# Kernel tuning notes

Hardware: AMD Instinct MI355X
Metric: run time of the kernel (lower is better)

The kernel has to match this reference:

```python
import jax, jax.numpy as jnp
import numpy as np

N_EMBD = 1024
N_HEAD = 16
HEAD_DIM = N_EMBD // N_HEAD  # 64
R = 8
D_STD = HEAD_DIM - R         # 56
BLOCK_SIZE = 2048
B, T = 2, 2048
NEG = -1e9


def setup_inputs() -> dict:
    key = jax.random.key(0)
    ks = jax.random.split(key, 8)
    x = jax.random.normal(ks[0], (B, T, N_EMBD), dtype=jnp.float32)
    Wqkv = jax.random.normal(ks[1], (3 * N_EMBD, N_EMBD), dtype=jnp.float32) * 0.02
    Wproj = jax.random.normal(ks[2], (N_EMBD, N_EMBD), dtype=jnp.float32) * 0.02
    W_recip = jax.random.normal(ks[3], (HEAD_DIM, R), dtype=jnp.float32) * 0.02
    # mixing weights must be positive (sqrt is taken); match init scale
    w_std = jnp.full((N_HEAD,), 0.5, dtype=jnp.float32)
    w_rec = jnp.full((N_HEAD,), 0.3, dtype=jnp.float32)  # > threshold -> all heads RA
    w_disc = jnp.full((N_HEAD,), 0.2, dtype=jnp.float32)
    d_bias = jax.random.normal(ks[4], (N_HEAD, BLOCK_SIZE), dtype=jnp.float32) * 0.02
    return {"x": x, "Wqkv": Wqkv, "Wproj": Wproj, "W_recip": W_recip,
            "w_std": w_std, "w_rec": w_rec, "w_disc": w_disc, "d_bias": d_bias}


def reference(x, Wqkv, Wproj, W_recip, w_std, w_rec, w_disc, d_bias):
    Bx, Tx, C = x.shape
    H, hd = N_HEAD, HEAD_DIM
    qkv = x @ Wqkv.T                                   # (B,T,3C)
    q, k, v = jnp.split(qkv, 3, axis=-1)
    def heads(t):
        return t.reshape(Bx, Tx, H, hd).transpose(0, 2, 1, 3)  # (B,H,T,hd)
    q, k, v = heads(q), heads(k), heads(v)
    q_low = jnp.einsum('bhtd,dr->bhtr', q, W_recip)    # (B,H,T,R)
    k_low = jnp.einsum('bhtd,dr->bhtr', k, W_recip)
    sw_std = jnp.sqrt(w_std)[None, :, None, None]
    sw_rec = jnp.sqrt(w_rec)[None, :, None, None]
    # cross augmentation: q side carries k_low, k side carries q_low
    q_aug = jnp.concatenate([sw_std * q[..., :D_STD], sw_rec * k_low], axis=-1)
    k_aug = jnp.concatenate([sw_std * k[..., :D_STD], sw_rec * q_low], axis=-1)
    scale = 1.0 / jnp.sqrt(jnp.asarray(hd, dtype=x.dtype))
    scores = jnp.einsum('bhqd,bhkd->bhqk', q_aug, k_aug) * scale
    # per-head learned bias over key positions, broadcast over queries
    bias = w_disc[None, :, None, None] * d_bias[:, :Tx][None, :, None, :]
    scores = scores + bias
    causal = jnp.tril(jnp.ones((Tx, Tx), dtype=bool))
    scores = jnp.where(causal[None, None], scores, NEG)
    attn = jax.nn.softmax(scores, axis=-1)
    out = jnp.einsum('bhqk,bhkd->bhqd', attn, v)       # (B,H,T,hd)
    out = out.transpose(0, 2, 1, 3).reshape(Bx, Tx, C)
    return out @ Wproj.T
```

## Files before the change

kernel.cpp:

```cpp
#include <hip/hip_runtime.h>
#include <math.h>

#define T_SEQ 2048
#define NH 16
#define HD 64
#define CEMB 1024
#define NEGINF -3.0e38f
#define LOG2E 1.4426950408889634f

typedef unsigned short ushort;
typedef unsigned int uint;
typedef __attribute__((ext_vector_type(8))) short short8;
typedef __attribute__((ext_vector_type(4))) float f32x4;

#if __has_builtin(__builtin_amdgcn_exp2f)
#define EXP2(x) __builtin_amdgcn_exp2f(x)
#else
#define EXP2(x) exp2f(x)
#endif

__device__ __forceinline__ float b2f(ushort h) {
    union { uint u; float f; } cv; cv.u = ((uint)h) << 16; return cv.f;
}
__device__ __forceinline__ ushort f2b(float f) {
    union { float f; uint u; } cv; cv.f = f;
    return (ushort)((cv.u + 0x7FFF + ((cv.u >> 16) & 1)) >> 16);
}
__device__ __forceinline__ ushort f2b_fast(float f) {
    union { float f; uint u; } cv; cv.f = f;
    return (ushort)((cv.u + 0x8000) >> 16);
}
__device__ __forceinline__ uint pack_bf16(float a, float b) {
    union { float f; uint u; } ua, ub; ua.f = a; ub.f = b;
    return __builtin_amdgcn_perm(ub.u + 0x8000u, ua.u + 0x8000u, 0x07060302u);
}
__device__ __forceinline__ void gl2lds16(const ushort* g, ushort* l) {
    __builtin_amdgcn_global_load_lds(
        (const __attribute__((address_space(1))) void*)g,
        (__attribute__((address_space(3))) void*)l, 16, 0, 0);
}

__global__ __launch_bounds__(256) void prep_kernel(
    const float* __restrict__ x, const float* __restrict__ Wqkv,
    const float* __restrict__ Wproj, const float* __restrict__ W_recip,
    const float* __restrict__ w_disc, const float* __restrict__ d_bias,
    ushort* __restrict__ xb, ushort* __restrict__ wqkvb,
    ushort* __restrict__ wprojb, float* __restrict__ bias_pre)
{
    const int bid = blockIdx.x;
    if (bid < 8192) {
        const float* src; ushort* dst; int off;
        if (bid < 4096)      { src = x;     dst = xb;     off = bid; }
        else if (bid < 7168) { src = Wqkv;  dst = wqkvb;  off = bid - 4096; }
        else                 { src = Wproj; dst = wprojb; off = bid - 7168; }
        const int i = (off * 256 + threadIdx.x) * 4;
        const float4 v = *(const float4*)&src[i];
        ushort4 o;
        o.x = f2b(v.x); o.y = f2b(v.y); o.z = f2b(v.z); o.w = f2b(v.w);
        *(ushort4*)&dst[i] = o;
        return;
    }
    if (bid >= 8224) {
        const int h = bid - 8224;
        const float wd = w_disc[h] * LOG2E;
        const int j = h * T_SEQ + threadIdx.x * 8;
        const float4 a = *(const float4*)&d_bias[j];
        const float4 c = *(const float4*)&d_bias[j + 4];
        float4 oa, oc;
        oa.x = a.x * wd; oa.y = a.y * wd; oa.z = a.z * wd; oa.w = a.w * wd;
        oc.x = c.x * wd; oc.y = c.y * wd; oc.z = c.z * wd; oc.w = c.w * wd;
        *(float4*)&bias_pre[j] = oa;
        *(float4*)&bias_pre[j + 4] = oc;
        return;
    }
    const int wb = bid - 8192;
    const int qk = wb >> 4, h = wb & 15;
    const int e0 = threadIdx.x * 4;
    f32x4 acc[8];
    #pragma unroll
    for (int r = 0; r < 8; ++r) acc[r] = (f32x4){0.f, 0.f, 0.f, 0.f};
    #pragma unroll 4
    for (int d = 0; d < 64; ++d) {
        const float4 xv = *(const float4*)&Wqkv[(size_t)(qk * 1024 + h * 64 + d) * 1024 + e0];
        #pragma unroll
        for (int r = 0; r < 8; ++r) {
            const float w = W_recip[d * 8 + r];
            acc[r][0] = fmaf(w, xv.x, acc[r][0]);
            acc[r][1] = fmaf(w, xv.y, acc[r][1]);
            acc[r][2] = fmaf(w, xv.z, acc[r][2]);
            acc[r][3] = fmaf(w, xv.w, acc[r][3]);
        }
    }
    #pragma unroll
    for (int r = 0; r < 8; ++r) {
        ushort4 o;
        o.x = f2b(acc[r][0]); o.y = f2b(acc[r][1]);
        o.z = f2b(acc[r][2]); o.w = f2b(acc[r][3]);
        *(ushort4*)&wqkvb[(size_t)(3072 + qk * 128 + h * 8 + r) * 1024 + e0] = o;
    }
}

#define GEMM_CORE(Aptr, Bptr, KDIM, SMEMN)                                     \
    __shared__ __align__(16) ushort SMEM[SMEMN];                               \
    ushort* const Asl = SMEM;                                                  \
    ushort* const Bsl = SMEM + 8192;                                           \
    const int row0 = blockIdx.x * 128;                                         \
    const int col0 = blockIdx.y * 128;                                         \
    const int tid = threadIdx.x;                                               \
    const int wave = tid >> 6, lane = tid & 63;                                \
    const int wm = wave >> 1, wn = wave & 1;                                   \
    const int quad = lane >> 4, lq = lane & 15;                                \
    const int l7 = lq & 7;                                                     \
    f32x4 acc[4][4];                                                           \
    _Pragma("unroll") for (int i = 0; i < 4; ++i)                              \
        _Pragma("unroll") for (int j = 0; j < 4; ++j)                          \
            acc[i][j] = (f32x4){0.f, 0.f, 0.f, 0.f};                           \
    for (int k0 = 0; k0 < (KDIM); k0 += 64) {                                  \
        _Pragma("unroll") for (int p = 0; p < 4; ++p) {                        \
            const int idx = p * 256 + tid;                                     \
            const int row = idx >> 3, slot = idx & 7;                          \
            const int kc = (slot ^ (row & 7)) << 3;                            \
            gl2lds16(&(Aptr)[(size_t)(row0 + row) * (KDIM) + k0 + kc], &Asl[idx * 8]); \
            gl2lds16(&(Bptr)[(size_t)(col0 + row) * (KDIM) + k0 + kc], &Bsl[idx * 8]); \
        }                                                                      \
        __syncthreads();                                                       \
        _Pragma("unroll") for (int ks = 0; ks < 2; ++ks) {                     \
            short8 af[4], bf[4];                                               \
            _Pragma("unroll") for (int i = 0; i < 4; ++i)                      \
                af[i] = *(const short8*)&Asl[(wm * 64 + i * 16 + lq) * 64 +    \
                                             (((ks * 4 + quad) ^ l7) << 3)];   \
            _Pragma("unroll") for (int j = 0; j < 4; ++j)                      \
                bf[j] = *(const short8*)&Bsl[(wn * 64 + j * 16 + lq) * 64 +    \
                                             (((ks * 4 + quad) ^ l7) << 3)];   \
            _Pragma("unroll") for (int i = 0; i < 4; ++i)                      \
                _Pragma("unroll") for (int j = 0; j < 4; ++j)                  \
                    acc[i][j] = __builtin_amdgcn_mfma_f32_16x16x32_bf16(       \
                        af[i], bf[j], acc[i][j], 0, 0, 0);                     \
        }                                                                      \
        __syncthreads();                                                       \
    }

#define CSTR 144
__global__ __launch_bounds__(256, 4) void gemm_qkv_kernel(
    const ushort* __restrict__ A, const ushort* __restrict__ Bt,
    const float* __restrict__ w_std, const float* __restrict__ w_rec,
    ushort* __restrict__ qh, ushort* __restrict__ kh, ushort* __restrict__ vt)
{
    GEMM_CORE(A, Bt, 1024, 128 * CSTR)
    ushort* const Cs = SMEM;

    if (col0 >= 2048 && col0 < 3072) {
        #pragma unroll
        for (int j = 0; j < 4; ++j) {
            const int cc = col0 + wn * 64 + j * 16 + lq;
            const int h = (cc >> 6) & 15;
            const int d = cc & 63;
            #pragma unroll
            for (int i = 0; i < 4; ++i) {
                const int rr0 = row0 + wm * 64 + i * 16 + quad * 4;
                const int b = rr0 >> 11, t0 = rr0 & 2047;
                ushort4 pv;
                pv.x = f2b(acc[i][j][0]); pv.y = f2b(acc[i][j][1]);
                pv.z = f2b(acc[i][j][2]); pv.w = f2b(acc[i][j][3]);
                *(ushort4*)&vt[((((size_t)b * NH + h) * HD + d) * T_SEQ + t0)] = pv;
            }
        }
    } else if (col0 < 2048) {
        const bool isq = (col0 < 1024);
        #pragma unroll
        for (int j = 0; j < 4; ++j) {
            const int colc = wn * 64 + j * 16 + lq;
            const int h = ((col0 + colc) >> 6) & 15;
            const float sc = isq ? w_std[h] * (0.125f * LOG2E) : 1.0f;
            #pragma unroll
            for (int i = 0; i < 4; ++i)
                #pragma unroll
                for (int r = 0; r < 4; ++r)
                    Cs[(wm * 64 + i * 16 + quad * 4 + r) * CSTR + colc] =
                        f2b(acc[i][j][r] * sc);
        }
        __syncthreads();
        ushort* dst = isq ? qh : kh;
        const int hbase = (col0 >> 6) & 15;
        #pragma unroll
        for (int rep = 0; rep < 8; ++rep) {
            const int id = rep * 256 + tid;
            const int row = id >> 4, chunk = id & 15;
            if ((chunk & 7) == 7) continue;
            const int h = hbase + (chunk >> 3);
            const int d = (chunk & 7) * 8;
            const int rr = row0 + row;
            const int b = rr >> 11, t = rr & 2047;
            const uint4 val = *(const uint4*)&Cs[row * CSTR + chunk * 8];
            *(uint4*)&dst[((((size_t)b * NH + h) * T_SEQ + t) * HD + d)] = val;
        }
    } else {
        const bool isqlow = (col0 < 3200);
        #pragma unroll
        for (int j = 0; j < 4; ++j) {
            const int colc = wn * 64 + j * 16 + lq;
            const int h = colc >> 3;
            const float sc = isqlow ? 1.0f : w_rec[h] * (0.125f * LOG2E);
            #pragma unroll
            for (int i = 0; i < 4; ++i)
                #pragma unroll
                for (int r = 0; r < 4; ++r)
                    Cs[(wm * 64 + i * 16 + quad * 4 + r) * CSTR + colc] =
                        f2b(acc[i][j][r] * sc);
        }
        __syncthreads();
        ushort* dst = isqlow ? kh : qh;
        #pragma unroll
        for (int rep = 0; rep < 8; ++rep) {
            const int id = rep * 256 + tid;
            const int row = id >> 4, h = id & 15;
            const int rr = row0 + row;
            const int b = rr >> 11, t = rr & 2047;
            const uint4 val = *(const uint4*)&Cs[row * CSTR + h * 8];
            *(uint4*)&dst[((((size_t)b * NH + h) * T_SEQ + t) * HD + 56)] = val;
        }
    }
}

__global__ __launch_bounds__(256, 4) void gemm_proj_kernel(
    const ushort* __restrict__ A, const ushort* __restrict__ Bt,
    float* __restrict__ C)
{
    GEMM_CORE(A, Bt, 1024, 16384)
    #pragma unroll
    for (int i = 0; i < 4; ++i) {
        #pragma unroll
        for (int r = 0; r < 4; ++r) {
            const int rr = row0 + wm * 64 + i * 16 + quad * 4 + r;
            #pragma unroll
            for (int j = 0; j < 4; ++j) {
                const int cc = col0 + wn * 64 + j * 16 + lq;
                C[(size_t)rr * 1024 + cc] = acc[i][j][r];
            }
        }
    }
}

#define TILE_COMPUTE(bq, o4, lsum, qrow, NTL) do {                            \
    f32x4 s4[8];                                                              \
    _Pragma("unroll") for (int nt = 0; nt < (NTL); ++nt)                      \
        s4[nt] = *(const f32x4*)&bias_h[k0 + nt * 16 + quad * 4];             \
    __builtin_amdgcn_s_setprio(1);                                            \
    _Pragma("unroll") for (int ks = 0; ks < 2; ++ks)                          \
        _Pragma("unroll") for (int nt = 0; nt < (NTL); ++nt) {                \
            const short8 ak = *(const short8*)                                \
                &Ks[(nt * 16 + lq) * 64 + (((ks * 4 + quad) ^ l7) << 3)];     \
            s4[nt] = __builtin_amdgcn_mfma_f32_16x16x32_bf16(                 \
                ak, (bq)[ks], s4[nt], 0, 0, 0);                               \
        }                                                                     \
    __builtin_amdgcn_s_setprio(0);                                            \
    _Pragma("unroll") for (int nt = 0; nt < (NTL); ++nt) {                    \
        f32x4 sv = s4[nt];                                                    \
        const int kb = k0 + nt * 16 + quad * 4;                               \
        _Pragma("unroll") for (int r = 0; r < 4; ++r)                         \
            if (kb + r > (qrow)) sv[r] = NEGINF;                              \
        const float p0 = EXP2(sv[0]), p1 = EXP2(sv[1]);                       \
        const float p2 = EXP2(sv[2]), p3 = EXP2(sv[3]);                       \
        (lsum) += (p0 + p1) + (p2 + p3);                                      \
        const int pcol = (nt * 16 + quad * 4) ^ (l7 << 3);                    \
        uint2 pv; pv.x = pack_bf16(p0, p1); pv.y = pack_bf16(p2, p3);         \
        *(uint2*)&Ps[prow + pcol] = pv;                                       \
    }                                                                         \
    __builtin_amdgcn_s_setprio(1);                                            \
    _Pragma("unroll") for (int ks = 0; ks < (NTL) / 2; ++ks) {                \
        const short8 bp = *(const short8*)                                    \
            &Ps[prow + ((ks * 32 + quad * 8) ^ (l7 << 3))];                   \
        _Pragma("unroll") for (int dt = 0; dt < 4; ++dt) {                    \
            const short8 bv = *(const short8*)                                \
                &Vs[(dt * 16 + lq) * 128 + (((ks * 4 + quad) ^ lq) << 3)];    \
            (o4)[dt] = __builtin_amdgcn_mfma_f32_16x16x32_bf16(               \
                bv, bp, (o4)[dt], 0, 0, 0);                                   \
        }                                                                     \
    }                                                                         \
    __builtin_amdgcn_s_setprio(0);                                            \
} while (0)

__global__ __launch_bounds__(256, 2) void attn_kernel(
    const ushort* __restrict__ qa, const ushort* __restrict__ ka,
    const ushort* __restrict__ vt, const float* __restrict__ bias_pre,
    ushort* __restrict__ out)
{
    __shared__ __align__(16) ushort Qs[2 * 64 * 64];
    __shared__ __align__(16) ushort Ks[128 * 64];
    __shared__ __align__(16) ushort Ps[64 * 128];
    __shared__ __align__(16) ushort Vs[64 * 128];
    const int bh = blockIdx.x;
    const int qtA = blockIdx.y;
    const int qtB = 31 - blockIdx.y;
    const int h = bh & 15, b = bh >> 4;
    const int tid = threadIdx.x;
    const int wave = tid >> 6, lane = tid & 63;
    const int quad = lane >> 4, lq = lane & 15;
    const int l7 = lq & 7;
    const size_t base = (size_t)bh * T_SEQ * HD;

    #pragma unroll
    for (int rep = 0; rep < 2; ++rep) {
        const int idx = rep * 256 + tid;
        const int row = idx >> 3, slot = idx & 7;
        const int kc = (slot ^ (row & 7)) << 3;
        gl2lds16(&qa[base + (size_t)(qtA * 64 + row) * 64 + kc], &Qs[idx * 8]);
        gl2lds16(&qa[base + (size_t)(qtB * 64 + row) * 64 + kc], &Qs[4096 + idx * 8]);
    }
    __syncthreads();
    short8 bqA[2], bqB[2];
    #pragma unroll
    for (int ks = 0; ks < 2; ++ks) {
        const int off = (wave * 16 + lq) * 64 + (((ks * 4 + quad) ^ l7) << 3);
        bqA[ks] = *(const short8*)&Qs[off];
        bqB[ks] = *(const short8*)&Qs[4096 + off];
    }

    f32x4 o4A[4], o4B[4];
    #pragma unroll
    for (int dt = 0; dt < 4; ++dt) {
        o4A[dt] = (f32x4){0.f, 0.f, 0.f, 0.f};
        o4B[dt] = (f32x4){0.f, 0.f, 0.f, 0.f};
    }
    float lsumA = 0.f, lsumB = 0.f;
    const int qrowA = qtA * 64 + wave * 16 + lq;
    const int qrowB = qtB * 64 + wave * 16 + lq;
    const int prow = (wave * 16 + lq) * 128;
    const int nA = (qtA + 2) >> 1, nB = (qtB + 2) >> 1;
    const float* bias_h = &bias_pre[h * T_SEQ];

    for (int c = 0; c < nB; ++c) {
        const int k0 = c * 128;
        if (c) __syncthreads();
        #pragma unroll
        for (int rep = 0; rep < 4; ++rep) {
            const int idx = rep * 256 + tid;
            const int row = idx >> 3, slot = idx & 7;
            gl2lds16(&ka[base + (size_t)(k0 + row) * 64 + ((slot ^ (row & 7)) << 3)],
                     &Ks[idx * 8]);
        }
        #pragma unroll
        for (int rep = 0; rep < 4; ++rep) {
            const int idx = rep * 256 + tid;
            const int row = idx >> 4, slot = idx & 15;
            gl2lds16(&vt[base + (size_t)row * T_SEQ + k0 + ((slot ^ (row & 15)) << 3)],
                     &Vs[idx * 8]);
        }
        __syncthreads();

        if (c == nB - 1 && !(qtB & 1)) TILE_COMPUTE(bqB, o4B, lsumB, qrowB, 4);
        else                           TILE_COMPUTE(bqB, o4B, lsumB, qrowB, 8);
        if (c < nA) {
            if (c == nA - 1 && !(qtA & 1)) TILE_COMPUTE(bqA, o4A, lsumA, qrowA, 4);
            else                           TILE_COMPUTE(bqA, o4A, lsumA, qrowA, 8);
        }
    }

    lsumA += __shfl_xor(lsumA, 16, 64);
    lsumA += __shfl_xor(lsumA, 32, 64);
    lsumB += __shfl_xor(lsumB, 16, 64);
    lsumB += __shfl_xor(lsumB, 32, 64);
    const float invA = 1.0f / lsumA, invB = 1.0f / lsumB;
    const size_t obaseA = ((size_t)b * T_SEQ + qrowA) * CEMB + h * HD;
    const size_t obaseB = ((size_t)b * T_SEQ + qrowB) * CEMB + h * HD;
    #pragma unroll
    for (int dt = 0; dt < 4; ++dt) {
        ushort4 ov;
        ov.x = f2b_fast(o4A[dt][0] * invA);
        ov.y = f2b_fast(o4A[dt][1] * invA);
        ov.z = f2b_fast(o4A[dt][2] * invA);
        ov.w = f2b_fast(o4A[dt][3] * invA);
        *(ushort4*)&out[obaseA + dt * 16 + quad * 4] = ov;
        ushort4 ow;
        ow.x = f2b_fast(o4B[dt][0] * invB);
        ow.y = f2b_fast(o4B[dt][1] * invB);
        ow.z = f2b_fast(o4B[dt][2] * invB);
        ow.w = f2b_fast(o4B[dt][3] * invB);
        *(ushort4*)&out[obaseB + dt * 16 + quad * 4] = ow;
    }
}

extern "C" void kernel_launch(void* const* d_in, const int* in_sizes, int n_in,
                              void* d_out, int out_size, void* d_ws, size_t ws_size,
                              hipStream_t stream) {
    const float* x       = (const float*)d_in[0];
    const float* Wqkv    = (const float*)d_in[1];
    const float* Wproj   = (const float*)d_in[2];
    const float* W_recip = (const float*)d_in[3];
    const float* w_std   = (const float*)d_in[4];
    const float* w_rec   = (const float*)d_in[5];
    const float* w_disc  = (const float*)d_in[6];
    const float* d_bias  = (const float*)d_in[7];
    float* out = (float*)d_out;

    const size_t NX = (size_t)4096 * 1024;
    const size_t NWQKVX = (size_t)3328 * 1024;
    const size_t NWPROJ = (size_t)1024 * 1024;
    ushort* xb     = (ushort*)d_ws;
    ushort* wqkvb  = xb + NX;
    ushort* wprojb = wqkvb + NWQKVX;
    ushort* qh     = wprojb + NWPROJ;
    ushort* kh     = qh + NX;
    ushort* vt     = kh + NX;
    ushort* ao     = vt + NX;
    float*  bias_pre = (float*)(ao + NX);

    prep_kernel<<<8240, 256, 0, stream>>>(x, Wqkv, Wproj, W_recip, w_disc, d_bias,
                                          xb, wqkvb, wprojb, bias_pre);
    gemm_qkv_kernel<<<dim3(32, 26), 256, 0, stream>>>(xb, wqkvb, w_std, w_rec, qh, kh, vt);
    attn_kernel<<<dim3(32, 16), 256, 0, stream>>>(qh, kh, vt, bias_pre, ao);
    gemm_proj_kernel<<<dim3(32, 8), 256, 0, stream>>>(ao, wprojb, out);
}
```

Measured before the change: 188.6 us.

## Shrink projection GEMM tile to 128x64 and launch low-rank prep blocks first

The output projection GEMM gets its own 128x64 tile loop in place of the shared 128x128 core. The grid doubles to 512 blocks so more of the GPU's compute units are busy on this 4096x1024x1024 GEMM. Each wave now computes a 32x64 slab, which lowers register pressure but reduces reuse of the B tile. Separately, the prep kernel's block order is changed so the slow low-rank weight-fold blocks and the bias blocks get the lowest block IDs and start before the bulk fp32-to-bf16 cast blocks, shortening the tail.

```diff
diff --git a/kernel.cpp b/kernel.cpp
--- a/kernel.cpp
+++ b/kernel.cpp
@@ -48,11 +48,12 @@
     ushort* __restrict__ wprojb, float* __restrict__ bias_pre)
 {
     const int bid = blockIdx.x;
-    if (bid < 8192) {
+    if (bid >= 48) {
+        const int off0 = bid - 48;
         const float* src; ushort* dst; int off;
-        if (bid < 4096)      { src = x;     dst = xb;     off = bid; }
-        else if (bid < 7168) { src = Wqkv;  dst = wqkvb;  off = bid - 4096; }
-        else                 { src = Wproj; dst = wprojb; off = bid - 7168; }
+        if (off0 < 4096)      { src = x;     dst = xb;     off = off0; }
+        else if (off0 < 7168) { src = Wqkv;  dst = wqkvb;  off = off0 - 4096; }
+        else                  { src = Wproj; dst = wprojb; off = off0 - 7168; }
         const int i = (off * 256 + threadIdx.x) * 4;
         const float4 v = *(const float4*)&src[i];
         ushort4 o;
@@ -60,8 +61,8 @@
         *(ushort4*)&dst[i] = o;
         return;
     }
-    if (bid >= 8224) {
-        const int h = bid - 8224;
+    if (bid >= 32) {
+        const int h = bid - 32;
         const float wd = w_disc[h] * LOG2E;
         const int j = h * T_SEQ + threadIdx.x * 8;
         const float4 a = *(const float4*)&d_bias[j];
@@ -73,8 +74,7 @@
         *(float4*)&bias_pre[j + 4] = oc;
         return;
     }
-    const int wb = bid - 8192;
-    const int qk = wb >> 4, h = wb & 15;
+    const int qk = bid >> 4, h = bid & 15;
     const int e0 = threadIdx.x * 4;
     f32x4 acc[8];
     #pragma unroll
@@ -226,15 +226,66 @@
     const ushort* __restrict__ A, const ushort* __restrict__ Bt,
     float* __restrict__ C)
 {
-    GEMM_CORE(A, Bt, 1024, 16384)
-    #pragma unroll
-    for (int i = 0; i < 4; ++i) {
+    __shared__ __align__(16) ushort SMEM[12288];
+    ushort* const Asl = SMEM;
+    ushort* const Bsl = SMEM + 8192;
+    const int row0 = blockIdx.x * 128;
+    const int col0 = blockIdx.y * 64;
+    const int tid = threadIdx.x;
+    const int wave = tid >> 6, lane = tid & 63;
+    const int quad = lane >> 4, lq = lane & 15;
+    const int l7 = lq & 7;
+    f32x4 acc[2][4];
+    #pragma unroll
+    for (int i = 0; i < 2; ++i)
+        #pragma unroll
+        for (int j = 0; j < 4; ++j)
+            acc[i][j] = (f32x4){0.f, 0.f, 0.f, 0.f};
+
+    for (int k0 = 0; k0 < 1024; k0 += 64) {
+        #pragma unroll
+        for (int p = 0; p < 4; ++p) {
+            const int idx = p * 256 + tid;
+            const int row = idx >> 3, slot = idx & 7;
+            const int kc = (slot ^ (row & 7)) << 3;
+            gl2lds16(&A[(size_t)(row0 + row) * 1024 + k0 + kc], &Asl[idx * 8]);
+        }
+        #pragma unroll
+        for (int p = 0; p < 2; ++p) {
+            const int idx = p * 256 + tid;
+            const int row = idx >> 3, slot = idx & 7;
+            const int kc = (slot ^ (row & 7)) << 3;
+            gl2lds16(&Bt[(size_t)(col0 + row) * 1024 + k0 + kc], &Bsl[idx * 8]);
+        }
+        __syncthreads();
+        #pragma unroll
+        for (int ks = 0; ks < 2; ++ks) {
+            short8 af[2], bf[4];
+            #pragma unroll
+            for (int i = 0; i < 2; ++i)
+                af[i] = *(const short8*)&Asl[(wave * 32 + i * 16 + lq) * 64 +
+                                             (((ks * 4 + quad) ^ l7) << 3)];
+            #pragma unroll
+            for (int j = 0; j < 4; ++j)
+                bf[j] = *(const short8*)&Bsl[(j * 16 + lq) * 64 +
+                                             (((ks * 4 + quad) ^ l7) << 3)];
+            #pragma unroll
+            for (int i = 0; i < 2; ++i)
+                #pragma unroll
+                for (int j = 0; j < 4; ++j)
+                    acc[i][j] = __builtin_amdgcn_mfma_f32_16x16x32_bf16(
+                        af[i], bf[j], acc[i][j], 0, 0, 0);
+        }
+        __syncthreads();
+    }
+    #pragma unroll
+    for (int i = 0; i < 2; ++i) {
         #pragma unroll
         for (int r = 0; r < 4; ++r) {
-            const int rr = row0 + wm * 64 + i * 16 + quad * 4 + r;
+            const int rr = row0 + wave * 32 + i * 16 + quad * 4 + r;
             #pragma unroll
             for (int j = 0; j < 4; ++j) {
-                const int cc = col0 + wn * 64 + j * 16 + lq;
+                const int cc = col0 + j * 16 + lq;
                 C[(size_t)rr * 1024 + cc] = acc[i][j][r];
             }
         }
@@ -409,5 +460,5 @@
                                           xb, wqkvb, wprojb, bias_pre);
     gemm_qkv_kernel<<<dim3(32, 26), 256, 0, stream>>>(xb, wqkvb, w_std, w_rec, qh, kh, vt);
     attn_kernel<<<dim3(32, 16), 256, 0, stream>>>(qh, kh, vt, bias_pre, ao);
-    gemm_proj_kernel<<<dim3(32, 8), 256, 0, stream>>>(ao, wprojb, out);
-}
+    gemm_proj_kernel<<<dim3(32, 16), 256, 0, stream>>>(ao, wprojb, out);
+}
```

Result: faster. 180.9 us (-4.1%).
